# Optimization experiments

Hardware: AMD Instinct MI355X
Metric: run time of the kernel (lower is better)

The kernel has to match this reference:

```python
import jax, jax.numpy as jnp
import numpy as np

N_NODES = 50000
N_EDGES = 640000
N_GRAPHS = 64
D_IN = 3
D_H = 128
N_CLASSES = 10
EPS = 1e-5


def setup_inputs() -> dict:
    key = jax.random.key(0)
    ks = jax.random.split(key, 32)
    inp = {
        "x": jax.random.normal(ks[0], (N_NODES, D_IN), dtype=jnp.float32),
        "src": jax.random.randint(ks[1], (N_EDGES,), 0, N_NODES, dtype=jnp.int32),
        "dst": jax.random.randint(ks[2], (N_EDGES,), 0, N_NODES, dtype=jnp.int32),
        "batch": jnp.sort(jax.random.randint(ks[3], (N_NODES,), 0, N_GRAPHS, dtype=jnp.int32)),
        "enc_w": jax.random.normal(ks[4], (D_IN, D_H), dtype=jnp.float32) * 0.1,
        "enc_b": jnp.zeros((D_H,), jnp.float32),
        "fc_w": jax.random.normal(ks[5], (D_H, D_H), dtype=jnp.float32) * 0.05,
        "fc_b": jnp.zeros((D_H,), jnp.float32),
        "pred_w": jax.random.normal(ks[6], (D_H, N_CLASSES), dtype=jnp.float32) * 0.05,
        "pred_b": jnp.zeros((N_CLASSES,), jnp.float32),
    }
    for i in range(4):
        inp[f"w{i}"] = jax.random.normal(ks[8 + i], (D_H, D_H), dtype=jnp.float32) * 0.05
        inp[f"b{i}"] = jnp.zeros((D_H,), jnp.float32)
        inp[f"ln_w{i}"] = jnp.ones((D_H,), jnp.float32)
        inp[f"ln_b{i}"] = jnp.zeros((D_H,), jnp.float32)
    return inp


def _gcn_norm(src, dst, n):
    # add self-loops, symmetric deg^{-1/2} normalization (GCNConv default)
    loop = jnp.arange(n, dtype=src.dtype)
    src_f = jnp.concatenate([src, loop])
    dst_f = jnp.concatenate([dst, loop])
    deg = jax.ops.segment_sum(jnp.ones_like(dst_f, jnp.float32), dst_f, num_segments=n)
    dinv = jnp.where(deg > 0, 1.0 / jnp.sqrt(deg), 0.0)
    norm = dinv[src_f] * dinv[dst_f]
    return src_f, dst_f, norm


def _gcn(x, w, b, src_f, dst_f, norm, n):
    h = x @ w                           # [N, D]
    m = h[src_f] * norm[:, None]        # gather + scale  [E+N, D]
    return jax.ops.segment_sum(m, dst_f, num_segments=n) + b


def _graph_ln(x, w, b):
    # PyG LayerNorm mode='graph', batch=None: normalize over ALL nodes+channels
    mu = x.mean()
    sd = jnp.sqrt(((x - mu) ** 2).mean())
    return (x - mu) / (sd + EPS) * w + b


def reference(x, src, dst, batch, enc_w, enc_b, fc_w, fc_b, pred_w, pred_b,
              w0, b0, ln_w0, ln_b0, w1, b1, ln_w1, ln_b1,
              w2, b2, ln_w2, ln_b2, w3, b3, ln_w3, ln_b3):
    n = x.shape[0]
    src_f, dst_f, norm = _gcn_norm(src, dst, n)
    h = jax.nn.elu(x @ enc_w + enc_b)   # input encoder (Linear + ELU)
    convs = [(w0, b0, ln_w0, ln_b0), (w1, b1, ln_w1, ln_b1),
             (w2, b2, ln_w2, ln_b2), (w3, b3, ln_w3, ln_b3)]
    for w, b, lw, lb in convs:
        h = _gcn(h, w, b, src_f, dst_f, norm, n)
        h = jax.nn.relu(h)
        h = _graph_ln(h, lw, lb)
    g = jax.ops.segment_max(h, batch, num_segments=N_GRAPHS)  # global_max_pool
    g = jnp.tanh(g @ fc_w + fc_b)
    return g @ pred_w + pred_b
```

## Files before the change

### kernel.cpp

```cpp
#include <hip/hip_runtime.h>
#include <cfloat>
#include <cmath>

#define D 128
#define D4 32
#define LB 32

typedef __attribute__((ext_vector_type(8))) short short8;
typedef __attribute__((ext_vector_type(4))) float f32x4;

__device__ __forceinline__ float4 f4fma(float s, float4 a, float4 acc) {
    acc.x = fmaf(s, a.x, acc.x);
    acc.y = fmaf(s, a.y, acc.y);
    acc.z = fmaf(s, a.z, acc.z);
    acc.w = fmaf(s, a.w, acc.w);
    return acc;
}

__device__ __forceinline__ unsigned short f2bf(float x) {
    unsigned int b = __float_as_uint(x);
    unsigned int r = (b + 0x7FFFu + ((b >> 16) & 1u)) >> 16;
    return (unsigned short)r;
}

__device__ __forceinline__ unsigned int pack2bf(float a, float b) {
    return (unsigned int)f2bf(a) | ((unsigned int)f2bf(b) << 16);
}

__device__ __forceinline__ float bf2f(unsigned short u) {
    return __uint_as_float(((unsigned int)u) << 16);
}

__device__ __forceinline__ void accum8(float* a, float nrm, uint4 t) {
    a[0] = fmaf(nrm, bf2f((unsigned short)(t.x & 0xFFFFu)), a[0]);
    a[1] = fmaf(nrm, bf2f((unsigned short)(t.x >> 16)), a[1]);
    a[2] = fmaf(nrm, bf2f((unsigned short)(t.y & 0xFFFFu)), a[2]);
    a[3] = fmaf(nrm, bf2f((unsigned short)(t.y >> 16)), a[3]);
    a[4] = fmaf(nrm, bf2f((unsigned short)(t.z & 0xFFFFu)), a[4]);
    a[5] = fmaf(nrm, bf2f((unsigned short)(t.z >> 16)), a[5]);
    a[6] = fmaf(nrm, bf2f((unsigned short)(t.w & 0xFFFFu)), a[6]);
    a[7] = fmaf(nrm, bf2f((unsigned short)(t.w >> 16)), a[7]);
}

__global__ void k_count(const int* __restrict__ dst, int* __restrict__ cnt, int E) {
    int i = blockIdx.x * blockDim.x + threadIdx.x;
    if (i < E) atomicAdd(&cnt[dst[i]], 1);
}

__global__ void k_scanall(const int* __restrict__ cnt, int* __restrict__ rowptr,
                          int* __restrict__ cur, float* __restrict__ dinv,
                          int N, int NB) {
    __shared__ int pre[256];
    int b = blockIdx.x, t = threadIdx.x;
    int limit = b * 256;
    int s = 0;
    for (int i = t; i < limit; i += 256) s += cnt[i];
    pre[t] = s;
    __syncthreads();
    for (int off = 128; off; off >>= 1) {
        if (t < off) pre[t] += pre[t + off];
        __syncthreads();
    }
    int base = pre[0];
    __syncthreads();
    int i = b * 256 + t;
    int v = (i < N) ? cnt[i] : 0;
    pre[t] = v;
    __syncthreads();
    for (int off = 1; off < 256; off <<= 1) {
        int u = (t >= off) ? pre[t - off] : 0;
        __syncthreads();
        pre[t] += u;
        __syncthreads();
    }
    if (i < N) {
        int excl = base + ((t == 0) ? 0 : pre[t - 1]);
        rowptr[i] = excl;
        cur[i] = excl;
        dinv[i] = 1.0f / sqrtf((float)v + 1.0f);
    }
    if (b == NB - 1 && t == 255) rowptr[N] = base + pre[255];
}

__global__ void k_fill(const int* __restrict__ src, const int* __restrict__ dst,
                       const float* __restrict__ dinv, int* __restrict__ cur,
                       int2* __restrict__ edata, int E) {
    int e = blockIdx.x * blockDim.x + threadIdx.x;
    if (e >= E) return;
    int s = src[e], d = dst[e];
    int p = atomicAdd(&cur[d], 1);
    edata[p] = make_int2(s, __float_as_int(dinv[s] * dinv[d]));
}

__global__ void k_enc(const float* __restrict__ x, const float* __restrict__ w,
                      const float* __restrict__ b, unsigned short* __restrict__ h, int N) {
    int idx = blockIdx.x * blockDim.x + threadIdx.x;
    if (idx >= N * D4) return;
    int n = idx >> 5, c4 = idx & 31;
    const float4* w4 = (const float4*)w;
    float4 b4 = ((const float4*)b)[c4];
    float x0 = x[n * 3 + 0], x1 = x[n * 3 + 1], x2 = x[n * 3 + 2];
    float4 v = b4;
    v = f4fma(x0, w4[0 * D4 + c4], v);
    v = f4fma(x1, w4[1 * D4 + c4], v);
    v = f4fma(x2, w4[2 * D4 + c4], v);
    v.x = v.x > 0.f ? v.x : expm1f(v.x);
    v.y = v.y > 0.f ? v.y : expm1f(v.y);
    v.z = v.z > 0.f ? v.z : expm1f(v.z);
    v.w = v.w > 0.f ? v.w : expm1f(v.w);
    ushort4 o;
    o.x = f2bf(v.x); o.y = f2bf(v.y); o.z = f2bf(v.z); o.w = f2bf(v.w);
    ((ushort4*)h)[idx] = o;
}

__global__ void k_prep(const float* __restrict__ w, const float* __restrict__ lw,
                       const float* __restrict__ lb, const double* __restrict__ sums,
                       unsigned short* __restrict__ wt, float* __restrict__ konst, int N) {
    __shared__ float sc[D], of[D];
    float mu = 0.f, inv = 1.f;
    if (lw) {
        double M = (double)N * D;
        double m = sums[0] / M;
        double var = sums[1] / M - m * m;
        float sd = sqrtf(var > 0.0 ? (float)var : 0.f);
        inv = 1.f / (sd + 1e-5f);
        mu = (float)m;
    }
    for (int i = threadIdx.x; i < D; i += blockDim.x) {
        float l = lw ? lw[i] : 1.f;
        float s = inv * l;
        sc[i] = s;
        of[i] = (lw ? lb[i] : 0.f) - mu * s;
    }
    __syncthreads();
    if (blockIdx.x < 8) {
        int nl = threadIdx.x & 15;
        int ck = threadIdx.x >> 4;
        int n = blockIdx.x * 16 + nl;
        unsigned int p[4];
        #pragma unroll
        for (int q = 0; q < 4; ++q) {
            int k0 = ck * 8 + 2 * q;
            float v0 = sc[k0 + 0] * w[(k0 + 0) * D + n];
            float v1 = sc[k0 + 1] * w[(k0 + 1) * D + n];
            p[q] = pack2bf(v0, v1);
        }
        uint4 u = make_uint4(p[0], p[1], p[2], p[3]);
        ((uint4*)(wt + (size_t)n * D))[ck] = u;
    } else {
        for (int j = threadIdx.x; j < D; j += blockDim.x) {
            float acc = 0.f;
            for (int c = 0; c < D; ++c) acc = fmaf(of[c], w[c * D + j], acc);
            konst[j] = acc;
        }
    }
}

__launch_bounds__(256)
__global__ void k_layer(const unsigned short* __restrict__ Ain,
                        const unsigned short* __restrict__ wt,
                        const float* __restrict__ konst, const float* __restrict__ bias,
                        const int2* __restrict__ edata, const int* __restrict__ rowptr,
                        const float* __restrict__ dinv,
                        unsigned short* __restrict__ Aout,
                        double* __restrict__ sums, int N) {
    __shared__ uint4 a_lds4[512];
    __shared__ float rs[LB];
    __shared__ float ss[4], sq[4];
    char* a_lds = (char*)a_lds4;
    int row0 = blockIdx.x * LB;

    int g = threadIdx.x >> 4;
    int lane = threadIdx.x & 15;
    const uint4* T16 = (const uint4*)Ain;
    for (int k = 0; k < 2; ++k) {
        int nl = g * 2 + k;
        int n = row0 + nl;
        if (n < N) {
            int e0 = rowptr[n], e1 = rowptr[n + 1];
            float acc[8];
            #pragma unroll
            for (int q = 0; q < 8; ++q) acc[q] = 0.f;
            float rsum = 0.f;
            int e = e0;
            for (; e + 8 <= e1; e += 8) {
                int2 ed[8]; uint4 tv[8];
                #pragma unroll
                for (int j = 0; j < 8; ++j) ed[j] = edata[e + j];
                #pragma unroll
                for (int j = 0; j < 8; ++j) tv[j] = T16[(size_t)ed[j].x * 16 + lane];
                #pragma unroll
                for (int j = 0; j < 8; ++j) {
                    float nm = __int_as_float(ed[j].y);
                    accum8(acc, nm, tv[j]);
                    rsum += nm;
                }
            }
            for (; e + 4 <= e1; e += 4) {
                int2 ed[4]; uint4 tv[4];
                #pragma unroll
                for (int j = 0; j < 4; ++j) ed[j] = edata[e + j];
                #pragma unroll
                for (int j = 0; j < 4; ++j) tv[j] = T16[(size_t)ed[j].x * 16 + lane];
                #pragma unroll
                for (int j = 0; j < 4; ++j) {
                    float nm = __int_as_float(ed[j].y);
                    accum8(acc, nm, tv[j]);
                    rsum += nm;
                }
            }
            for (; e < e1; ++e) {
                int2 d = edata[e];
                float nm = __int_as_float(d.y);
                accum8(acc, nm, T16[(size_t)d.x * 16 + lane]);
                rsum += nm;
            }
            float di = dinv[n];
            float sl = di * di;
            accum8(acc, sl, T16[(size_t)n * 16 + lane]);
            rsum += sl;
            int i = nl * 16 + lane;
            int byte = (i << 4) ^ ((nl & 7) << 4);
            *(uint4*)(a_lds + byte) = make_uint4(pack2bf(acc[0], acc[1]),
                                                 pack2bf(acc[2], acc[3]),
                                                 pack2bf(acc[4], acc[5]),
                                                 pack2bf(acc[6], acc[7]));
            if (lane == 0) rs[nl] = rsum;
        }
    }
    __syncthreads();

    int wv = threadIdx.x >> 6;
    int l64 = threadIdx.x & 63;
    int lrow = l64 & 15;
    int kg = l64 >> 4;
    int rt = wv & 1;
    int cb = wv >> 1;

    f32x4 acc2[4];
    #pragma unroll
    for (int ct = 0; ct < 4; ++ct) acc2[ct] = (f32x4){0.f, 0.f, 0.f, 0.f};

    #pragma unroll
    for (int ks = 0; ks < 4; ++ks) {
        int ar = rt * 16 + lrow;
        int abyte = (ar * 256 + ks * 64 + kg * 16) ^ ((ar & 7) << 4);
        short8 a = *(short8*)(a_lds + abyte);
        #pragma unroll
        for (int ct = 0; ct < 4; ++ct) {
            int col = cb * 64 + ct * 16 + lrow;
            short8 b = *(const short8*)(wt + (size_t)col * D + ks * 32 + kg * 8);
            acc2[ct] = __builtin_amdgcn_mfma_f32_16x16x32_bf16(a, b, acc2[ct], 0, 0, 0);
        }
    }

    float ls = 0.f, lq = 0.f;
    #pragma unroll
    for (int ct = 0; ct < 4; ++ct) {
        int col = cb * 64 + ct * 16 + lrow;
        float kc = konst[col];
        float bb = bias[col];
        #pragma unroll
        for (int r = 0; r < 4; ++r) {
            int rtile = rt * 16 + kg * 4 + r;
            int row = row0 + rtile;
            if (row < N) {
                float v = acc2[ct][r] + rs[rtile] * kc + bb;
                v = fmaxf(v, 0.f);
                Aout[(size_t)row * D + col] = f2bf(v);
                ls += v;
                lq += v * v;
            }
        }
    }
    for (int off = 32; off; off >>= 1) {
        ls += __shfl_down(ls, off);
        lq += __shfl_down(lq, off);
    }
    if (l64 == 0) { ss[wv] = ls; sq[wv] = lq; }
    __syncthreads();
    if (threadIdx.x == 0) {
        float S = ss[0] + ss[1] + ss[2] + ss[3];
        float Q = sq[0] + sq[1] + sq[2] + sq[3];
        atomicAdd(&sums[0], (double)S);
        atomicAdd(&sums[1], (double)Q);
    }
}

__launch_bounds__(512)
__global__ void k_tail(const unsigned short* __restrict__ A, const int* __restrict__ batch,
                       const float* __restrict__ lw, const float* __restrict__ lb,
                       const double* __restrict__ sums,
                       const float* __restrict__ fc_w, const float* __restrict__ fc_b,
                       const float* __restrict__ pred_w, const float* __restrict__ pred_b,
                       float* __restrict__ out, int N) {
    int gi = blockIdx.x;
    int lo = 0, hi = N;
    while (lo < hi) { int mid = (lo + hi) >> 1; if (batch[mid] < gi) lo = mid + 1; else hi = mid; }
    int start = lo;
    hi = N;
    while (lo < hi) { int mid = (lo + hi) >> 1; if (batch[mid] < gi + 1) lo = mid + 1; else hi = mid; }
    int end = lo;

    int c = threadIdx.x & 127, sub = threadIdx.x >> 7;
    double M = (double)N * D;
    double m_ = sums[0] / M;
    double var = sums[1] / M - m_ * m_;
    float sd = sqrtf(var > 0.0 ? (float)var : 0.f);
    float inv = 1.f / (sd + 1e-5f);
    float s = inv * lw[c];
    float o = lb[c] - (float)m_ * s;

    float mx = -FLT_MAX;
    for (int node = start + sub; node < end; node += 4)
        mx = fmaxf(mx, fmaf(bf2f(A[(size_t)node * D + c]), s, o));

    __shared__ float red[4][128];
    __shared__ float gm[128], tr[128];
    red[sub][c] = mx;
    __syncthreads();
    if (sub == 0)
        gm[c] = fmaxf(fmaxf(red[0][c], red[1][c]), fmaxf(red[2][c], red[3][c]));
    __syncthreads();
    if (threadIdx.x < 128) {
        float acc = fc_b[c];
        for (int k = 0; k < D; ++k) acc = fmaf(gm[k], fc_w[k * D + c], acc);
        tr[c] = tanhf(acc);
    }
    __syncthreads();
    if (threadIdx.x < 10) {
        int j = threadIdx.x;
        float acc = pred_b[j];
        for (int k = 0; k < D; ++k) acc = fmaf(tr[k], pred_w[k * 10 + j], acc);
        out[gi * 10 + j] = acc;
    }
}

extern "C" void kernel_launch(void* const* d_in, const int* in_sizes, int n_in,
                              void* d_out, int out_size, void* d_ws, size_t ws_size,
                              hipStream_t stream) {
    const float* x      = (const float*)d_in[0];
    const int*   src    = (const int*)d_in[1];
    const int*   dst    = (const int*)d_in[2];
    const int*   batch  = (const int*)d_in[3];
    const float* enc_w  = (const float*)d_in[4];
    const float* enc_b  = (const float*)d_in[5];
    const float* fc_w   = (const float*)d_in[6];
    const float* fc_b   = (const float*)d_in[7];
    const float* pred_w = (const float*)d_in[8];
    const float* pred_b = (const float*)d_in[9];

    int N = in_sizes[0] / 3;
    int E = in_sizes[1];
    int G = out_size / 10;
    int NB = (N + 255) / 256;

    char* ws = (char*)d_ws;
    size_t off = 0;
    auto align512 = [](size_t v) { return (v + 511) / 512 * 512; };
    int*   cnt    = (int*)(ws + off);   off += align512((size_t)N * 4);
    double* sums  = (double*)(ws + off); off += 512;
    float* dinv   = (float*)(ws + off); off += align512((size_t)N * 4);
    int*   rowptr = (int*)(ws + off);   off += align512(((size_t)N + 1) * 4);
    int*   cur    = (int*)(ws + off);   off += align512((size_t)N * 4);
    int2*  edata  = (int2*)(ws + off);  off += align512((size_t)E * 8);
    unsigned short* A0 = (unsigned short*)(ws + off); off += align512((size_t)N * D * 2);
    unsigned short* A1 = (unsigned short*)(ws + off); off += align512((size_t)N * D * 2);
    unsigned short* wt = (unsigned short*)(ws + off); off += align512((size_t)D * D * 2);
    float* konst  = (float*)(ws + off); off += align512((size_t)D * 4);

    hipMemsetAsync(cnt, 0, align512((size_t)N * 4) + 512, stream);
    k_count<<<(E + 255) / 256, 256, 0, stream>>>(dst, cnt, E);
    k_scanall<<<NB, 256, 0, stream>>>(cnt, rowptr, cur, dinv, N, NB);
    k_fill<<<(E + 255) / 256, 256, 0, stream>>>(src, dst, dinv, cur, edata, E);

    int tot4 = N * D4;
    k_enc<<<(tot4 + 255) / 256, 256, 0, stream>>>(x, enc_w, enc_b, A0, N);

    int NBL = (N + LB - 1) / LB;
    unsigned short* Ain = A0;
    unsigned short* Aout = A1;
    for (int L = 0; L < 4; ++L) {
        const float* w  = (const float*)d_in[10 + 4 * L];
        const float* b  = (const float*)d_in[11 + 4 * L];
        const float* lwp = L ? (const float*)d_in[12 + 4 * (L - 1)] : nullptr;
        const float* lbp = L ? (const float*)d_in[13 + 4 * (L - 1)] : nullptr;
        k_prep<<<9, 256, 0, stream>>>(w, lwp, lbp, &sums[2 * (L ? L - 1 : 0)], wt, konst, N);
        k_layer<<<NBL, 256, 0, stream>>>(Ain, wt, konst, b, edata, rowptr, dinv,
                                         Aout, &sums[2 * L], N);
        unsigned short* tmp = Ain; Ain = Aout; Aout = tmp;
    }

    const float* lw3 = (const float*)d_in[12 + 4 * 3];
    const float* lb3 = (const float*)d_in[13 + 4 * 3];
    k_tail<<<G, 512, 0, stream>>>(Ain, batch, lw3, lb3, &sums[6],
                                  fc_w, fc_b, pred_w, pred_b, (float*)d_out, N);
}
```

Before: 540.1 us.

## Merge encoder and degree count kernels, deepen gather unroll to 16 edges

Combines the input encoder and the edge-degree counting atomics into one launch, with block ranges picking the role, which removes one kernel launch and lets the two run concurrently. The aggregation loop in the layer kernel now issues two batches of 8 row gathers before accumulating, giving 16 loads in flight per iteration. The 4-edge remainder loop becomes a single optional 8-edge block followed by the scalar tail. Keeping 16 uint4 loads live raises register pressure, which could lower occupancy.

```diff
diff --git a/kernel.cpp b/kernel.cpp
--- a/kernel.cpp
+++ b/kernel.cpp
@@ -42,9 +42,32 @@
     a[7] = fmaf(nrm, bf2f((unsigned short)(t.w >> 16)), a[7]);
 }
 
-__global__ void k_count(const int* __restrict__ dst, int* __restrict__ cnt, int E) {
-    int i = blockIdx.x * blockDim.x + threadIdx.x;
-    if (i < E) atomicAdd(&cnt[dst[i]], 1);
+__global__ void k_pre(const float* __restrict__ x, const float* __restrict__ ew,
+                      const float* __restrict__ eb, unsigned short* __restrict__ h,
+                      const int* __restrict__ dst, int* __restrict__ cnt,
+                      int N, int E, int EB) {
+    if ((int)blockIdx.x < EB) {
+        int idx = blockIdx.x * 256 + threadIdx.x;
+        if (idx >= N * D4) return;
+        int n = idx >> 5, c4 = idx & 31;
+        const float4* w4 = (const float4*)ew;
+        float4 b4 = ((const float4*)eb)[c4];
+        float x0 = x[n * 3 + 0], x1 = x[n * 3 + 1], x2 = x[n * 3 + 2];
+        float4 v = b4;
+        v = f4fma(x0, w4[0 * D4 + c4], v);
+        v = f4fma(x1, w4[1 * D4 + c4], v);
+        v = f4fma(x2, w4[2 * D4 + c4], v);
+        v.x = v.x > 0.f ? v.x : expm1f(v.x);
+        v.y = v.y > 0.f ? v.y : expm1f(v.y);
+        v.z = v.z > 0.f ? v.z : expm1f(v.z);
+        v.w = v.w > 0.f ? v.w : expm1f(v.w);
+        ushort4 o;
+        o.x = f2bf(v.x); o.y = f2bf(v.y); o.z = f2bf(v.z); o.w = f2bf(v.w);
+        ((ushort4*)h)[idx] = o;
+    } else {
+        int i = (blockIdx.x - EB) * 256 + threadIdx.x;
+        if (i < E) atomicAdd(&cnt[dst[i]], 1);
+    }
 }
 
 __global__ void k_scanall(const int* __restrict__ cnt, int* __restrict__ rowptr,
@@ -90,27 +113,6 @@
     int s = src[e], d = dst[e];
     int p = atomicAdd(&cur[d], 1);
     edata[p] = make_int2(s, __float_as_int(dinv[s] * dinv[d]));
-}
-
-__global__ void k_enc(const float* __restrict__ x, const float* __restrict__ w,
-                      const float* __restrict__ b, unsigned short* __restrict__ h, int N) {
-    int idx = blockIdx.x * blockDim.x + threadIdx.x;
-    if (idx >= N * D4) return;
-    int n = idx >> 5, c4 = idx & 31;
-    const float4* w4 = (const float4*)w;
-    float4 b4 = ((const float4*)b)[c4];
-    float x0 = x[n * 3 + 0], x1 = x[n * 3 + 1], x2 = x[n * 3 + 2];
-    float4 v = b4;
-    v = f4fma(x0, w4[0 * D4 + c4], v);
-    v = f4fma(x1, w4[1 * D4 + c4], v);
-    v = f4fma(x2, w4[2 * D4 + c4], v);
-    v.x = v.x > 0.f ? v.x : expm1f(v.x);
-    v.y = v.y > 0.f ? v.y : expm1f(v.y);
-    v.z = v.z > 0.f ? v.z : expm1f(v.z);
-    v.w = v.w > 0.f ? v.w : expm1f(v.w);
-    ushort4 o;
-    o.x = f2bf(v.x); o.y = f2bf(v.y); o.z = f2bf(v.z); o.w = f2bf(v.w);
-    ((ushort4*)h)[idx] = o;
 }
 
 __global__ void k_prep(const float* __restrict__ w, const float* __restrict__ lw,
@@ -183,27 +185,42 @@
             for (int q = 0; q < 8; ++q) acc[q] = 0.f;
             float rsum = 0.f;
             int e = e0;
-            for (; e + 8 <= e1; e += 8) {
-                int2 ed[8]; uint4 tv[8];
-                #pragma unroll
-                for (int j = 0; j < 8; ++j) ed[j] = edata[e + j];
-                #pragma unroll
-                for (int j = 0; j < 8; ++j) tv[j] = T16[(size_t)ed[j].x * 16 + lane];
+            int nb = (e1 - e0) >> 3;
+            int npair = nb >> 1;
+            for (int p = 0; p < npair; ++p) {
+                int2 edA[8]; uint4 tvA[8];
+                int2 edB[8]; uint4 tvB[8];
+                #pragma unroll
+                for (int j = 0; j < 8; ++j) edA[j] = edata[e + j];
+                #pragma unroll
+                for (int j = 0; j < 8; ++j) tvA[j] = T16[(size_t)edA[j].x * 16 + lane];
+                #pragma unroll
+                for (int j = 0; j < 8; ++j) edB[j] = edata[e + 8 + j];
+                #pragma unroll
+                for (int j = 0; j < 8; ++j) tvB[j] = T16[(size_t)edB[j].x * 16 + lane];
+                e += 16;
                 #pragma unroll
                 for (int j = 0; j < 8; ++j) {
-                    float nm = __int_as_float(ed[j].y);
-                    accum8(acc, nm, tv[j]);
+                    float nm = __int_as_float(edA[j].y);
+                    accum8(acc, nm, tvA[j]);
+                    rsum += nm;
+                }
+                #pragma unroll
+                for (int j = 0; j < 8; ++j) {
+                    float nm = __int_as_float(edB[j].y);
+                    accum8(acc, nm, tvB[j]);
                     rsum += nm;
                 }
             }
-            for (; e + 4 <= e1; e += 4) {
-                int2 ed[4]; uint4 tv[4];
-                #pragma unroll
-                for (int j = 0; j < 4; ++j) ed[j] = edata[e + j];
-                #pragma unroll
-                for (int j = 0; j < 4; ++j) tv[j] = T16[(size_t)ed[j].x * 16 + lane];
-                #pragma unroll
-                for (int j = 0; j < 4; ++j) {
+            if (nb & 1) {
+                int2 ed[8]; uint4 tv[8];
+                #pragma unroll
+                for (int j = 0; j < 8; ++j) ed[j] = edata[e + j];
+                #pragma unroll
+                for (int j = 0; j < 8; ++j) tv[j] = T16[(size_t)ed[j].x * 16 + lane];
+                e += 8;
+                #pragma unroll
+                for (int j = 0; j < 8; ++j) {
                     float nm = __int_as_float(ed[j].y);
                     accum8(acc, nm, tv[j]);
                     rsum += nm;
@@ -370,12 +387,11 @@
     float* konst  = (float*)(ws + off); off += align512((size_t)D * 4);
 
     hipMemsetAsync(cnt, 0, align512((size_t)N * 4) + 512, stream);
-    k_count<<<(E + 255) / 256, 256, 0, stream>>>(dst, cnt, E);
+    int EB = (N * D4 + 255) / 256;
+    int CB = (E + 255) / 256;
+    k_pre<<<EB + CB, 256, 0, stream>>>(x, enc_w, enc_b, A0, dst, cnt, N, E, EB);
     k_scanall<<<NB, 256, 0, stream>>>(cnt, rowptr, cur, dinv, N, NB);
     k_fill<<<(E + 255) / 256, 256, 0, stream>>>(src, dst, dinv, cur, edata, E);
-
-    int tot4 = N * D4;
-    k_enc<<<(tot4 + 255) / 256, 256, 0, stream>>>(x, enc_w, enc_b, A0, N);
 
     int NBL = (N + LB - 1) / LB;
     unsigned short* Ain = A0;
```

After: 619.6 us. +14.7%, slower.

## Fold graph LayerNorm into aggregation and merge prep kernels into one launch

Applied to the files above, without the earlier changes.

Removes the per-layer k_prep launches. The LayerNorm scale and offset from the previous layer are now computed inside k_layer and applied to the aggregated rows before the bf16 MFMA, so the weights no longer need rescaling and can be converted to bf16 once, for all four layers, up front. The encoder, degree count and weight conversion are merged into a single k_pre launch. This cuts four small serialized launches per forward pass and the konst matvec, at the cost of redundant per-block stat computation and a slightly different rounding point for the normalization.

```diff
diff --git a/kernel.cpp b/kernel.cpp
--- a/kernel.cpp
+++ b/kernel.cpp
@@ -42,9 +42,51 @@
     a[7] = fmaf(nrm, bf2f((unsigned short)(t.w >> 16)), a[7]);
 }
 
-__global__ void k_count(const int* __restrict__ dst, int* __restrict__ cnt, int E) {
-    int i = blockIdx.x * blockDim.x + threadIdx.x;
-    if (i < E) atomicAdd(&cnt[dst[i]], 1);
+__global__ void k_pre(const float* __restrict__ x, const float* __restrict__ ew,
+                      const float* __restrict__ eb, unsigned short* __restrict__ h,
+                      const int* __restrict__ dst, int* __restrict__ cnt,
+                      const float* __restrict__ w0, const float* __restrict__ w1,
+                      const float* __restrict__ w2, const float* __restrict__ w3,
+                      unsigned short* __restrict__ wt,
+                      int N, int E, int EB, int CB) {
+    int b = blockIdx.x;
+    if (b < EB) {
+        int idx = b * 256 + threadIdx.x;
+        if (idx >= N * D4) return;
+        int n = idx >> 5, c4 = idx & 31;
+        const float4* w4 = (const float4*)ew;
+        float4 b4 = ((const float4*)eb)[c4];
+        float x0 = x[n * 3 + 0], x1 = x[n * 3 + 1], x2 = x[n * 3 + 2];
+        float4 v = b4;
+        v = f4fma(x0, w4[0 * D4 + c4], v);
+        v = f4fma(x1, w4[1 * D4 + c4], v);
+        v = f4fma(x2, w4[2 * D4 + c4], v);
+        v.x = v.x > 0.f ? v.x : expm1f(v.x);
+        v.y = v.y > 0.f ? v.y : expm1f(v.y);
+        v.z = v.z > 0.f ? v.z : expm1f(v.z);
+        v.w = v.w > 0.f ? v.w : expm1f(v.w);
+        ushort4 o;
+        o.x = f2bf(v.x); o.y = f2bf(v.y); o.z = f2bf(v.z); o.w = f2bf(v.w);
+        ((ushort4*)h)[idx] = o;
+    } else if (b < EB + CB) {
+        int i = (b - EB) * 256 + threadIdx.x;
+        if (i < E) atomicAdd(&cnt[dst[i]], 1);
+    } else {
+        int bb = b - EB - CB;
+        int l = bb >> 3, blk = bb & 7;
+        const float* w = (l == 0) ? w0 : (l == 1) ? w1 : (l == 2) ? w2 : w3;
+        unsigned short* wtl = wt + (size_t)l * D * D;
+        int nl = threadIdx.x & 15;
+        int ck = threadIdx.x >> 4;
+        int n = blk * 16 + nl;
+        unsigned int p[4];
+        #pragma unroll
+        for (int q = 0; q < 4; ++q) {
+            int k0 = ck * 8 + 2 * q;
+            p[q] = pack2bf(w[(k0 + 0) * D + n], w[(k0 + 1) * D + n]);
+        }
+        ((uint4*)(wtl + (size_t)n * D))[ck] = make_uint4(p[0], p[1], p[2], p[3]);
+    }
 }
 
 __global__ void k_scanall(const int* __restrict__ cnt, int* __restrict__ rowptr,
@@ -92,83 +134,37 @@
     edata[p] = make_int2(s, __float_as_int(dinv[s] * dinv[d]));
 }
 
-__global__ void k_enc(const float* __restrict__ x, const float* __restrict__ w,
-                      const float* __restrict__ b, unsigned short* __restrict__ h, int N) {
-    int idx = blockIdx.x * blockDim.x + threadIdx.x;
-    if (idx >= N * D4) return;
-    int n = idx >> 5, c4 = idx & 31;
-    const float4* w4 = (const float4*)w;
-    float4 b4 = ((const float4*)b)[c4];
-    float x0 = x[n * 3 + 0], x1 = x[n * 3 + 1], x2 = x[n * 3 + 2];
-    float4 v = b4;
-    v = f4fma(x0, w4[0 * D4 + c4], v);
-    v = f4fma(x1, w4[1 * D4 + c4], v);
-    v = f4fma(x2, w4[2 * D4 + c4], v);
-    v.x = v.x > 0.f ? v.x : expm1f(v.x);
-    v.y = v.y > 0.f ? v.y : expm1f(v.y);
-    v.z = v.z > 0.f ? v.z : expm1f(v.z);
-    v.w = v.w > 0.f ? v.w : expm1f(v.w);
-    ushort4 o;
-    o.x = f2bf(v.x); o.y = f2bf(v.y); o.z = f2bf(v.z); o.w = f2bf(v.w);
-    ((ushort4*)h)[idx] = o;
-}
-
-__global__ void k_prep(const float* __restrict__ w, const float* __restrict__ lw,
-                       const float* __restrict__ lb, const double* __restrict__ sums,
-                       unsigned short* __restrict__ wt, float* __restrict__ konst, int N) {
-    __shared__ float sc[D], of[D];
-    float mu = 0.f, inv = 1.f;
-    if (lw) {
-        double M = (double)N * D;
-        double m = sums[0] / M;
-        double var = sums[1] / M - m * m;
-        float sd = sqrtf(var > 0.0 ? (float)var : 0.f);
-        inv = 1.f / (sd + 1e-5f);
-        mu = (float)m;
-    }
-    for (int i = threadIdx.x; i < D; i += blockDim.x) {
-        float l = lw ? lw[i] : 1.f;
-        float s = inv * l;
-        sc[i] = s;
-        of[i] = (lw ? lb[i] : 0.f) - mu * s;
-    }
-    __syncthreads();
-    if (blockIdx.x < 8) {
-        int nl = threadIdx.x & 15;
-        int ck = threadIdx.x >> 4;
-        int n = blockIdx.x * 16 + nl;
-        unsigned int p[4];
-        #pragma unroll
-        for (int q = 0; q < 4; ++q) {
-            int k0 = ck * 8 + 2 * q;
-            float v0 = sc[k0 + 0] * w[(k0 + 0) * D + n];
-            float v1 = sc[k0 + 1] * w[(k0 + 1) * D + n];
-            p[q] = pack2bf(v0, v1);
-        }
-        uint4 u = make_uint4(p[0], p[1], p[2], p[3]);
-        ((uint4*)(wt + (size_t)n * D))[ck] = u;
-    } else {
-        for (int j = threadIdx.x; j < D; j += blockDim.x) {
-            float acc = 0.f;
-            for (int c = 0; c < D; ++c) acc = fmaf(of[c], w[c * D + j], acc);
-            konst[j] = acc;
-        }
-    }
-}
-
 __launch_bounds__(256)
 __global__ void k_layer(const unsigned short* __restrict__ Ain,
                         const unsigned short* __restrict__ wt,
-                        const float* __restrict__ konst, const float* __restrict__ bias,
+                        const float* __restrict__ lwp, const float* __restrict__ lbp,
+                        const double* __restrict__ sums_prev,
+                        const float* __restrict__ bias,
                         const int2* __restrict__ edata, const int* __restrict__ rowptr,
                         const float* __restrict__ dinv,
                         unsigned short* __restrict__ Aout,
                         double* __restrict__ sums, int N) {
     __shared__ uint4 a_lds4[512];
-    __shared__ float rs[LB];
+    __shared__ float s_sh[D], o_sh[D];
     __shared__ float ss[4], sq[4];
     char* a_lds = (char*)a_lds4;
     int row0 = blockIdx.x * LB;
+
+    if (threadIdx.x < D) {
+        float s = 1.f, o = 0.f;
+        if (lwp) {
+            double M = (double)N * D;
+            double m = sums_prev[0] / M;
+            double var = sums_prev[1] / M - m * m;
+            float sd = sqrtf(var > 0.0 ? (float)var : 0.f);
+            float inv = 1.f / (sd + 1e-5f);
+            s = inv * lwp[threadIdx.x];
+            o = lbp[threadIdx.x] - (float)m * s;
+        }
+        s_sh[threadIdx.x] = s;
+        o_sh[threadIdx.x] = o;
+    }
+    __syncthreads();
 
     int g = threadIdx.x >> 4;
     int lane = threadIdx.x & 15;
@@ -219,13 +215,18 @@
             float sl = di * di;
             accum8(acc, sl, T16[(size_t)n * 16 + lane]);
             rsum += sl;
+            float v[8];
+            #pragma unroll
+            for (int q = 0; q < 8; ++q) {
+                int ch = 8 * lane + q;
+                v[q] = fmaf(s_sh[ch], acc[q], rsum * o_sh[ch]);
+            }
             int i = nl * 16 + lane;
             int byte = (i << 4) ^ ((nl & 7) << 4);
-            *(uint4*)(a_lds + byte) = make_uint4(pack2bf(acc[0], acc[1]),
-                                                 pack2bf(acc[2], acc[3]),
-                                                 pack2bf(acc[4], acc[5]),
-                                                 pack2bf(acc[6], acc[7]));
-            if (lane == 0) rs[nl] = rsum;
+            *(uint4*)(a_lds + byte) = make_uint4(pack2bf(v[0], v[1]),
+                                                 pack2bf(v[2], v[3]),
+                                                 pack2bf(v[4], v[5]),
+                                                 pack2bf(v[6], v[7]));
         }
     }
     __syncthreads();
@@ -258,14 +259,13 @@
     #pragma unroll
     for (int ct = 0; ct < 4; ++ct) {
         int col = cb * 64 + ct * 16 + lrow;
-        float kc = konst[col];
         float bb = bias[col];
         #pragma unroll
         for (int r = 0; r < 4; ++r) {
             int rtile = rt * 16 + kg * 4 + r;
             int row = row0 + rtile;
             if (row < N) {
-                float v = acc2[ct][r] + rs[rtile] * kc + bb;
+                float v = acc2[ct][r] + bb;
                 v = fmaxf(v, 0.f);
                 Aout[(size_t)row * D + col] = f2bf(v);
                 ls += v;
@@ -366,33 +366,38 @@
     int2*  edata  = (int2*)(ws + off);  off += align512((size_t)E * 8);
     unsigned short* A0 = (unsigned short*)(ws + off); off += align512((size_t)N * D * 2);
     unsigned short* A1 = (unsigned short*)(ws + off); off += align512((size_t)N * D * 2);
-    unsigned short* wt = (unsigned short*)(ws + off); off += align512((size_t)D * D * 2);
-    float* konst  = (float*)(ws + off); off += align512((size_t)D * 4);
+    unsigned short* wt = (unsigned short*)(ws + off); off += align512((size_t)4 * D * D * 2);
+
+    const float* wL[4], *bL[4], *lwL[4], *lbL[4];
+    for (int L = 0; L < 4; ++L) {
+        wL[L]  = (const float*)d_in[10 + 4 * L];
+        bL[L]  = (const float*)d_in[11 + 4 * L];
+        lwL[L] = (const float*)d_in[12 + 4 * L];
+        lbL[L] = (const float*)d_in[13 + 4 * L];
+    }
 
     hipMemsetAsync(cnt, 0, align512((size_t)N * 4) + 512, stream);
-    k_count<<<(E + 255) / 256, 256, 0, stream>>>(dst, cnt, E);
+    int EB = (N * D4 + 255) / 256;
+    int CB = (E + 255) / 256;
+    k_pre<<<EB + CB + 32, 256, 0, stream>>>(x, enc_w, enc_b, A0, dst, cnt,
+                                            wL[0], wL[1], wL[2], wL[3], wt,
+                                            N, E, EB, CB);
     k_scanall<<<NB, 256, 0, stream>>>(cnt, rowptr, cur, dinv, N, NB);
     k_fill<<<(E + 255) / 256, 256, 0, stream>>>(src, dst, dinv, cur, edata, E);
-
-    int tot4 = N * D4;
-    k_enc<<<(tot4 + 255) / 256, 256, 0, stream>>>(x, enc_w, enc_b, A0, N);
 
     int NBL = (N + LB - 1) / LB;
     unsigned short* Ain = A0;
     unsigned short* Aout = A1;
     for (int L = 0; L < 4; ++L) {
-        const float* w  = (const float*)d_in[10 + 4 * L];
-        const float* b  = (const float*)d_in[11 + 4 * L];
-        const float* lwp = L ? (const float*)d_in[12 + 4 * (L - 1)] : nullptr;
-        const float* lbp = L ? (const float*)d_in[13 + 4 * (L - 1)] : nullptr;
-        k_prep<<<9, 256, 0, stream>>>(w, lwp, lbp, &sums[2 * (L ? L - 1 : 0)], wt, konst, N);
-        k_layer<<<NBL, 256, 0, stream>>>(Ain, wt, konst, b, edata, rowptr, dinv,
+        const float* lwp = L ? lwL[L - 1] : nullptr;
+        const float* lbp = L ? lbL[L - 1] : nullptr;
+        k_layer<<<NBL, 256, 0, stream>>>(Ain, wt + (size_t)L * D * D,
+                                         lwp, lbp, &sums[2 * (L ? L - 1 : 0)],
+                                         bL[L], edata, rowptr, dinv,
                                          Aout, &sums[2 * L], N);
         unsigned short* tmp = Ain; Ain = Aout; Aout = tmp;
     }
 
-    const float* lw3 = (const float*)d_in[12 + 4 * 3];
-    const float* lb3 = (const float*)d_in[13 + 4 * 3];
-    k_tail<<<G, 512, 0, stream>>>(Ain, batch, lw3, lb3, &sums[6],
+    k_tail<<<G, 512, 0, stream>>>(Ain, batch, lwL[3], lbL[3], &sums[6],
                                   fc_w, fc_b, pred_w, pred_b, (float*)d_out, N);
 }
```

New measurement: 529.1 us. 2.0% less time.
